# Optimization experiments

Hardware: AMD Instinct MI355X
Metric: run time of the kernel (lower is better)

Reference implementation:

```python
import math
import jax, jax.numpy as jnp
import numpy as np

B = 512
E = 512
C = 70722
M_MARGIN = 0.4
H = 0.333
S = 64.0
T_ALPHA = 1.0
EPS = 1e-3


def setup_inputs() -> dict:
    key = jax.random.key(0)
    k1, k2, k3, k4 = jax.random.split(key, 4)
    embbedings = jax.random.normal(k1, (B, E), dtype=jnp.float32)
    embbedings = embbedings / jnp.linalg.norm(embbedings, axis=1, keepdims=True)
    # feature norms typically ~[10, 30] for face models
    norms = 10.0 + 20.0 * jax.random.uniform(k2, (B, 1), dtype=jnp.float32)
    label = jax.random.randint(k3, (B,), 0, C, dtype=jnp.int64)
    kernel = jax.random.normal(k4, (E, C), dtype=jnp.float32)
    batch_mean = jnp.ones((C,), dtype=jnp.float32) * 20.0
    batch_std = jnp.asarray(10.0, dtype=jnp.float32)
    return {"embbedings": embbedings, "norms": norms, "label": label,
            "kernel": kernel, "batch_mean": batch_mean, "batch_std": batch_std}


def reference(embbedings, norms, label, kernel, batch_mean, batch_std):
    # column-wise l2-normalize the class weight matrix [E, C]
    kernel_norm = kernel / jnp.linalg.norm(kernel, axis=0, keepdims=True)
    cosine = jnp.clip(embbedings @ kernel_norm, -1.0 + EPS, 1.0 - EPS)  # [B, C]
    safe_norms = jnp.clip(norms, 1e-3, 100.0)  # [B, 1]

    # ---- running-stat update (torch.no_grad block) ----
    sn = jax.lax.stop_gradient(safe_norms[:, 0])  # [B]
    sums = jnp.zeros((C,), dtype=sn.dtype).at[label].add(sn)
    counts = jnp.zeros((C,), dtype=sn.dtype).at[label].add(1.0)
    group_mean = sums / jnp.maximum(counts, 1.0)  # per-class batch mean of norms
    new_mean = jnp.where(counts > 0,
                         group_mean * T_ALPHA + (1.0 - T_ALPHA) * batch_mean,
                         batch_mean)
    std = jnp.std(sn, ddof=1)  # torch.std is unbiased
    new_std = std * T_ALPHA + (1.0 - T_ALPHA) * batch_std

    # ---- adaptive margin ----
    margin_scaler = (safe_norms - new_mean[label][:, None]) / (new_std + EPS)
    margin_scaler = jnp.clip(margin_scaler * H, -1.0, 1.0)  # [B, 1]

    oh = jax.nn.one_hot(label, C, dtype=cosine.dtype)  # [B, C]
    g_angular = -M_MARGIN * margin_scaler               # [B, 1]
    theta = jnp.arccos(cosine)
    theta_m = jnp.clip(theta + oh * g_angular, EPS, math.pi - EPS)
    g_add = M_MARGIN + M_MARGIN * margin_scaler         # [B, 1]
    out = (jnp.cos(theta_m) - oh * g_add) * S
    return out
```

## Files before the change

kernel.cpp:

```cpp
#include <hip/hip_runtime.h>
#include <hip/hip_bf16.h>
#include <cstdint>
#include <cstddef>
#include <math.h>

#define B_SZ 512
#define E_SZ 512
#define C_SZ 70722
#define PAD_C 70784
#define M_MARGIN 0.4f
#define H_CONST 0.333f
#define S_CONST 64.0f
#define EPS_F 1e-3f
#define PI_F 3.14159265358979323846f

typedef __attribute__((ext_vector_type(8))) short short8;
typedef __attribute__((ext_vector_type(4))) float f32x4;


__device__ __forceinline__ unsigned short f2bf(float x) {
  __hip_bfloat16 h = __float2bfloat16(x);
  unsigned short u;
  __builtin_memcpy(&u, &h, 2);
  return u;
}

__device__ __forceinline__ void gload_lds16(const void* g, void* l) {
  __builtin_amdgcn_global_load_lds(
      (const __attribute__((address_space(1))) unsigned int*)g,
      (__attribute__((address_space(3))) unsigned int*)l, 16, 0, 0);
}

__device__ __forceinline__ int swzb(int rc) {
  return (((rc & 7) ^ ((rc >> 2) & 7)) << 4);
}

__global__ void k_stats(const float* __restrict__ norms, const int* __restrict__ label,
                        float* __restrict__ ga, float* __restrict__ gadd) {
  __shared__ float sn[B_SZ];
  __shared__ int lab[B_SZ];
  __shared__ float redA[8], redB[8];
  __shared__ float sh_std;

  int t = threadIdx.x;
  float v = norms[t];
  v = fminf(fmaxf(v, 1e-3f), 100.0f);
  sn[t] = v;
  lab[t] = label[t];

  float s1 = v, s2 = v * v;
  #pragma unroll
  for (int o = 32; o > 0; o >>= 1) {
    s1 += __shfl_down(s1, o);
    s2 += __shfl_down(s2, o);
  }
  if ((t & 63) == 0) { redA[t >> 6] = s1; redB[t >> 6] = s2; }
  __syncthreads();
  if (t == 0) {
    float a = 0.f, b = 0.f;
    #pragma unroll
    for (int i = 0; i < 8; ++i) { a += redA[i]; b += redB[i]; }
    float mean = a / (float)B_SZ;
    float var = (b - (float)B_SZ * mean * mean) / (float)(B_SZ - 1);
    sh_std = sqrtf(fmaxf(var, 0.f));
  }
  __syncthreads();
  float stdv = sh_std;

  int myl = lab[t];
  float s = 0.f, cnt = 0.f;
  for (int j = 0; j < B_SZ; ++j) {
    bool m = (lab[j] == myl);
    s += m ? sn[j] : 0.f;
    cnt += m ? 1.f : 0.f;
  }
  float gm = s / fmaxf(cnt, 1.f);
  float ms = (v - gm) / (stdv + EPS_F) * H_CONST;
  ms = fminf(fmaxf(ms, -1.f), 1.f);
  ga[t] = -M_MARGIN * ms;
  gadd[t] = M_MARGIN + M_MARGIN * ms;
}

__global__ void k_cvtA(const float* __restrict__ emb, unsigned short* __restrict__ abf) {
  int i = (blockIdx.x * 256 + threadIdx.x) * 4;
  float4 f = *(const float4*)(emb + i);
  unsigned short u0 = f2bf(f.x), u1 = f2bf(f.y), u2 = f2bf(f.z), u3 = f2bf(f.w);
  unsigned long long pk = (unsigned long long)u0 | ((unsigned long long)u1 << 16) |
                          ((unsigned long long)u2 << 32) | ((unsigned long long)u3 << 48);
  *(unsigned long long*)(abf + i) = pk;
}

__global__ void k_prep(const float* __restrict__ K, float* __restrict__ invn,
                       unsigned short* __restrict__ BT) {
  __shared__ float T[64 * 64];
  __shared__ float part[16][64];

  const int t = threadIdx.x;
  const int c0 = blockIdx.x * 64;
  const int cl = t & 15;
  const int kr = t >> 4;
  const int cq = t >> 2;
  const int kq = t & 3;
  const bool full = (c0 + 64 <= C_SZ);

  float ss0 = 0.f, ss1 = 0.f, ss2 = 0.f, ss3 = 0.f;

  for (int ch = 0; ch < 8; ++ch) {
    if (ch) __syncthreads();
    #pragma unroll
    for (int i = 0; i < 4; ++i) {
      int klo = kr + i * 16;
      int kg = ch * 64 + klo;
      float4 f;
      if (full) {
        f = *(const float4*)(K + (size_t)kg * C_SZ + c0 + cl * 4);
      } else {
        float* fp = (float*)&f;
        #pragma unroll
        for (int j = 0; j < 4; ++j) {
          int c = c0 + cl * 4 + j;
          fp[j] = (c < C_SZ) ? K[(size_t)kg * C_SZ + c] : 0.f;
        }
      }
      ss0 += f.x * f.x; ss1 += f.y * f.y; ss2 += f.z * f.z; ss3 += f.w * f.w;
      int swz = (klo & 7) << 2;
      *(float4*)&T[klo * 64 + ((cl * 4) ^ swz)] = f;
    }
    __syncthreads();
    #pragma unroll
    for (int sub = 0; sub < 2; ++sub) {
      int k8 = sub * 32 + kq * 8;
      short8 v;
      #pragma unroll
      for (int i = 0; i < 8; ++i) {
        v[i] = (short)f2bf(T[(k8 + i) * 64 + (cq ^ (i << 2))]);
      }
      *(short8*)(BT + ((size_t)(c0 + cq) << 9) + ch * 64 + k8) = v;
    }
  }

  __syncthreads();
  part[kr][cl * 4 + 0] = ss0;
  part[kr][cl * 4 + 1] = ss1;
  part[kr][cl * 4 + 2] = ss2;
  part[kr][cl * 4 + 3] = ss3;
  __syncthreads();
  if (t < 64) {
    int c = c0 + t;
    float s = 0.f;
    #pragma unroll
    for (int r = 0; r < 16; ++r) s += part[r][t];
    invn[c] = (c < C_SZ) ? rsqrtf(s) : 0.f;
  }
}

__launch_bounds__(256)
__global__ void k_gemm_fast(const unsigned short* __restrict__ Abf,
                            const unsigned short* __restrict__ BT,
                            const float* __restrict__ invn,
                            const int* __restrict__ label,
                            const float* __restrict__ ga,
                            const float* __restrict__ gadd,
                            float* __restrict__ out) {
  __shared__ __align__(16) unsigned short As[128 * 64];
  __shared__ __align__(16) unsigned short Bs[128 * 64];
  __shared__ int lab_s[128];
  __shared__ float ga_s[128], gadd_s[128];

  const int tid = threadIdx.x;
  const int nwg = gridDim.x;
  int bid = blockIdx.x;

  int q = nwg >> 3, r8 = nwg & 7;
  int xcd = bid & 7, lb = bid >> 3;
  int wg = (xcd < r8 ? xcd * (q + 1) : r8 * (q + 1) + (xcd - r8) * q) + lb;

  const int mt = wg & 3;
  const int nt = wg >> 2;
  const int row0 = mt << 7;
  const int col0 = nt << 7;

  if (tid < 128) {
    int gr = row0 + tid;
    lab_s[tid] = label[gr];
    ga_s[tid] = ga[gr];
    gadd_s[tid] = gadd[gr];
  }

  const int wid = tid >> 6, lane = tid & 63;
  const int wr = wid >> 1, wc = wid & 1;

  f32x4 acc[4][4];
  #pragma unroll
  for (int m = 0; m < 4; ++m)
    #pragma unroll
    for (int n = 0; n < 4; ++n)
      acc[m][n] = f32x4{0.f, 0.f, 0.f, 0.f};

  const int rsub = lane >> 3;
  const int lchunk = lane & 7;

  for (int kt = 0; kt < 8; ++kt) {
    const int kb = kt * 64;
    if (kt) __syncthreads();

    #pragma unroll
    for (int rr = 0; rr < 4; ++rr) {
      int rowblk = wid * 32 + rr * 8;
      int r = rowblk + rsub;
      int s = lchunk ^ ((r & 7) ^ ((r >> 2) & 7));
      gload_lds16(Abf + (size_t)(row0 + r) * 512 + kb + s * 8,
                  (char*)As + rowblk * 128);
      gload_lds16(BT + (size_t)(col0 + r) * 512 + kb + s * 8,
                  (char*)Bs + rowblk * 128);
    }

    __syncthreads();

    #pragma unroll
    for (int ks = 0; ks < 2; ++ks) {
      short8 a[4], b[4];
      #pragma unroll
      for (int m = 0; m < 4; ++m) {
        int row = wr * 64 + m * 16 + (lane & 15);
        int off = (row * 128 + ks * 64 + (lane >> 4) * 16) ^ swzb(row);
        a[m] = *(const short8*)((const char*)As + off);
      }
      #pragma unroll
      for (int n = 0; n < 4; ++n) {
        int c = wc * 64 + n * 16 + (lane & 15);
        int off = (c * 128 + ks * 64 + (lane >> 4) * 16) ^ swzb(c);
        b[n] = *(const short8*)((const char*)Bs + off);
      }
      #pragma unroll
      for (int m = 0; m < 4; ++m)
        #pragma unroll
        for (int n = 0; n < 4; ++n)
          acc[m][n] = __builtin_amdgcn_mfma_f32_16x16x32_bf16(a[m], b[n], acc[m][n], 0, 0, 0);
    }
  }

  float invc[4];
  #pragma unroll
  for (int n = 0; n < 4; ++n)
    invc[n] = invn[col0 + wc * 64 + n * 16 + (lane & 15)];

  #pragma unroll
  for (int m = 0; m < 4; ++m) {
    int rl0 = wr * 64 + m * 16 + ((lane >> 4) << 2);
    #pragma unroll
    for (int n = 0; n < 4; ++n) {
      int cl = wc * 64 + n * 16 + (lane & 15);
      int gc = col0 + cl;
      if (gc >= C_SZ) continue;
      #pragma unroll
      for (int r = 0; r < 4; ++r) {
        int rl = rl0 + r;
        float v = acc[m][n][r] * invc[n];
        v = fminf(fmaxf(v, -1.f + EPS_F), 1.f - EPS_F);
        float res = v * S_CONST;
        if (gc == lab_s[rl]) {
          float th = acosf(v) + ga_s[rl];
          th = fminf(fmaxf(th, EPS_F), PI_F - EPS_F);
          res = (cosf(th) - gadd_s[rl]) * S_CONST;
        }
        out[(size_t)(row0 + rl) * C_SZ + gc] = res;
      }
    }
  }
}


__global__ void k_colnorm(const float* __restrict__ K, float* __restrict__ inv) {
  __shared__ float part[4][64];
  int cl = threadIdx.x & 63;
  int rq = threadIdx.x >> 6;
  int c = blockIdx.x * 64 + cl;
  float s = 0.f;
  if (c < C_SZ) {
    const float* p = K + (size_t)rq * 128 * C_SZ + c;
    #pragma unroll 8
    for (int r = 0; r < 128; ++r) {
      float x = p[(size_t)r * C_SZ];
      s += x * x;
    }
  }
  part[rq][cl] = s;
  __syncthreads();
  if (threadIdx.x < 64) {
    int c2 = blockIdx.x * 64 + threadIdx.x;
    if (c2 < C_SZ) {
      float tt = part[0][threadIdx.x] + part[1][threadIdx.x] +
                 part[2][threadIdx.x] + part[3][threadIdx.x];
      inv[c2] = rsqrtf(tt);
    } else if (c2 < PAD_C) {
      inv[c2] = 0.f;
    }
  }
}

__launch_bounds__(256)
__global__ void k_gemm_fb(const unsigned short* __restrict__ Abf,
                          const float* __restrict__ Kmat,
                          const float* __restrict__ invn,
                          const int* __restrict__ label,
                          const float* __restrict__ ga,
                          const float* __restrict__ gadd,
                          float* __restrict__ out) {
  __shared__ __align__(16) unsigned short As[128 * 64];
  __shared__ __align__(16) unsigned short Bs[128 * 64];
  __shared__ int lab_s[128];
  __shared__ float ga_s[128], gadd_s[128];

  const int tid = threadIdx.x;
  const int nwg = gridDim.x;
  int bid = blockIdx.x;
  int q = nwg >> 3, r8 = nwg & 7;
  int xcd = bid & 7, lb = bid >> 3;
  int wg = (xcd < r8 ? xcd * (q + 1) : r8 * (q + 1) + (xcd - r8) * q) + lb;
  const int mt = wg & 3;
  const int nt = wg >> 2;
  const int row0 = mt << 7;
  const int col0 = nt << 7;

  if (tid < 128) {
    int gr = row0 + tid;
    lab_s[tid] = label[gr];
    ga_s[tid] = ga[gr];
    gadd_s[tid] = gadd[gr];
  }

  const int wid = tid >> 6, lane = tid & 63;
  const int wr = wid >> 1, wc = wid & 1;
  const int cc = tid & 31;
  const int kq = tid >> 5;
  const bool edge = (col0 + 128 > C_SZ);
  float4 inv4 = *(const float4*)(invn + col0 + cc * 4);

  f32x4 acc[4][4];
  #pragma unroll
  for (int m = 0; m < 4; ++m)
    #pragma unroll
    for (int n = 0; n < 4; ++n)
      acc[m][n] = f32x4{0.f, 0.f, 0.f, 0.f};

  const float* Bg = Kmat + col0;

  for (int kt = 0; kt < 8; ++kt) {
    const int kb = kt * 64;
    if (kt) __syncthreads();

    #pragma unroll
    for (int rr = 0; rr < 4; ++rr) {
      int rowblk = wid * 32 + rr * 8;
      int r = rowblk + (lane >> 3);
      int s = (lane & 7) ^ ((r & 7) ^ ((r >> 2) & 7));
      gload_lds16(Abf + (size_t)(row0 + r) * 512 + kb + s * 8, (char*)As + rowblk * 128);
    }

    #pragma unroll
    for (int i = 0; i < 4; ++i) {
      int k = (kq + i * 8) * 2;
      const float* g0 = Bg + (size_t)(kb + k) * C_SZ + cc * 4;
      const float* g1 = g0 + C_SZ;
      float x0[4], x1[4];
      if (!edge) {
        float4 f0 = *(const float4*)g0;
        float4 f1 = *(const float4*)g1;
        x0[0]=f0.x; x0[1]=f0.y; x0[2]=f0.z; x0[3]=f0.w;
        x1[0]=f1.x; x1[1]=f1.y; x1[2]=f1.z; x1[3]=f1.w;
      } else {
        #pragma unroll
        for (int j = 0; j < 4; ++j) {
          int gc = col0 + cc * 4 + j;
          x0[j] = (gc < C_SZ) ? g0[j] : 0.f;
          x1[j] = (gc < C_SZ) ? g1[j] : 0.f;
        }
      }
      #pragma unroll
      for (int j = 0; j < 4; ++j) {
        int c = cc * 4 + j;
        float iv = ((const float*)&inv4)[j];
        unsigned int pk = ((unsigned int)f2bf(x1[j] * iv) << 16) | (unsigned int)f2bf(x0[j] * iv);
        int byte = (c * 128 + k * 2) ^ swzb(c);
        *(unsigned int*)((char*)Bs + byte) = pk;
      }
    }

    __syncthreads();

    #pragma unroll
    for (int ks = 0; ks < 2; ++ks) {
      short8 a[4], b[4];
      #pragma unroll
      for (int m = 0; m < 4; ++m) {
        int row = wr * 64 + m * 16 + (lane & 15);
        int off = (row * 128 + ks * 64 + (lane >> 4) * 16) ^ swzb(row);
        a[m] = *(const short8*)((const char*)As + off);
      }
      #pragma unroll
      for (int n = 0; n < 4; ++n) {
        int c = wc * 64 + n * 16 + (lane & 15);
        int off = (c * 128 + ks * 64 + (lane >> 4) * 16) ^ swzb(c);
        b[n] = *(const short8*)((const char*)Bs + off);
      }
      #pragma unroll
      for (int m = 0; m < 4; ++m)
        #pragma unroll
        for (int n = 0; n < 4; ++n)
          acc[m][n] = __builtin_amdgcn_mfma_f32_16x16x32_bf16(a[m], b[n], acc[m][n], 0, 0, 0);
    }
  }

  #pragma unroll
  for (int m = 0; m < 4; ++m) {
    int rl0 = wr * 64 + m * 16 + ((lane >> 4) << 2);
    #pragma unroll
    for (int n = 0; n < 4; ++n) {
      int cl = wc * 64 + n * 16 + (lane & 15);
      int gc = col0 + cl;
      if (gc >= C_SZ) continue;
      #pragma unroll
      for (int r = 0; r < 4; ++r) {
        int rl = rl0 + r;
        float v = acc[m][n][r];
        v = fminf(fmaxf(v, -1.f + EPS_F), 1.f - EPS_F);
        float res = v * S_CONST;
        if (gc == lab_s[rl]) {
          float th = acosf(v) + ga_s[rl];
          th = fminf(fmaxf(th, EPS_F), PI_F - EPS_F);
          res = (cosf(th) - gadd_s[rl]) * S_CONST;
        }
        out[(size_t)(row0 + rl) * C_SZ + gc] = res;
      }
    }
  }
}

extern "C" void kernel_launch(void* const* d_in, const int* in_sizes, int n_in,
                              void* d_out, int out_size, void* d_ws, size_t ws_size,
                              hipStream_t stream) {
  const float* emb   = (const float*)d_in[0];
  const float* norms = (const float*)d_in[1];
  const int*   label = (const int*)d_in[2];
  const float* kmat  = (const float*)d_in[3];
  float* out = (float*)d_out;

  const size_t NEED_FAST = 73294336;
  char* ws = (char*)d_ws;
  float* invn = (float*)ws;
  float* ga   = (float*)(ws + 283136);
  float* gadd = (float*)(ws + 285184);
  unsigned short* abf = (unsigned short*)(ws + 287232);
  unsigned short* bt  = (unsigned short*)(ws + 811520);

  k_stats<<<1, 512, 0, stream>>>(norms, label, ga, gadd);
  k_cvtA<<<256, 256, 0, stream>>>(emb, abf);

  if (ws_size >= NEED_FAST) {
    k_prep<<<1106, 256, 0, stream>>>(kmat, invn, bt);
    k_gemm_fast<<<2212, 256, 0, stream>>>(abf, bt, invn, label, ga, gadd, out);
  } else {
    k_colnorm<<<1106, 256, 0, stream>>>(kmat, invn);
    k_gemm_fb<<<2212, 256, 0, stream>>>(abf, kmat, invn, label, ga, gadd, out);
  }
}
```

Measured before the change: 150.1 us.

## Triple-buffer LDS with BK=32 prefetch pipeline in fused GEMM kernel

```diff
diff --git a/kernel.cpp b/kernel.cpp
--- a/kernel.cpp
+++ b/kernel.cpp
@@ -162,8 +162,8 @@
                             const float* __restrict__ ga,
                             const float* __restrict__ gadd,
                             float* __restrict__ out) {
-  __shared__ __align__(16) unsigned short As[128 * 64];
-  __shared__ __align__(16) unsigned short Bs[128 * 64];
+  __shared__ __align__(16) unsigned short As[3][128 * 32];
+  __shared__ __align__(16) unsigned short Bs[3][128 * 32];
   __shared__ int lab_s[128];
   __shared__ float ga_s[128], gadd_s[128];
 
@@ -190,6 +190,31 @@
   const int wid = tid >> 6, lane = tid & 63;
   const int wr = wid >> 1, wc = wid & 1;
 
+  const int lr = lane >> 2;
+  const int lc = lane & 3;
+  const int rA0 = wid * 32 + lr;
+  const int rA1 = wid * 32 + 16 + lr;
+  const int sA0 = lc ^ ((rA0 >> 1) & 3);
+  const int sA1 = lc ^ ((rA1 >> 1) & 3);
+  const unsigned short* srcA0 = Abf + (size_t)(row0 + rA0) * 512 + sA0 * 8;
+  const unsigned short* srcA1 = Abf + (size_t)(row0 + rA1) * 512 + sA1 * 8;
+  const unsigned short* srcB0 = BT + (size_t)(col0 + rA0) * 512 + sA0 * 8;
+  const unsigned short* srcB1 = BT + (size_t)(col0 + rA1) * 512 + sA1 * 8;
+  char* const dA0 = (char*)&As[0][0] + (wid * 32) * 64;
+  char* const dB0 = (char*)&Bs[0][0] + (wid * 32) * 64;
+
+  int offA[4], offB[4];
+  #pragma unroll
+  for (int m = 0; m < 4; ++m) {
+    int row = wr * 64 + m * 16 + (lane & 15);
+    offA[m] = row * 64 + (((lane >> 4) ^ ((row >> 1) & 3)) << 4);
+  }
+  #pragma unroll
+  for (int n = 0; n < 4; ++n) {
+    int cr = wc * 64 + n * 16 + (lane & 15);
+    offB[n] = cr * 64 + (((lane >> 4) ^ ((cr >> 1) & 3)) << 4);
+  }
+
   f32x4 acc[4][4];
   #pragma unroll
   for (int m = 0; m < 4; ++m)
@@ -197,48 +222,54 @@
     for (int n = 0; n < 4; ++n)
       acc[m][n] = f32x4{0.f, 0.f, 0.f, 0.f};
 
-  const int rsub = lane >> 3;
-  const int lchunk = lane & 7;
-
-  for (int kt = 0; kt < 8; ++kt) {
-    const int kb = kt * 64;
-    if (kt) __syncthreads();
-
-    #pragma unroll
-    for (int rr = 0; rr < 4; ++rr) {
-      int rowblk = wid * 32 + rr * 8;
-      int r = rowblk + rsub;
-      int s = lchunk ^ ((r & 7) ^ ((r >> 2) & 7));
-      gload_lds16(Abf + (size_t)(row0 + r) * 512 + kb + s * 8,
-                  (char*)As + rowblk * 128);
-      gload_lds16(BT + (size_t)(col0 + r) * 512 + kb + s * 8,
-                  (char*)Bs + rowblk * 128);
-    }
-
-    __syncthreads();
-
-    #pragma unroll
-    for (int ks = 0; ks < 2; ++ks) {
-      short8 a[4], b[4];
-      #pragma unroll
-      for (int m = 0; m < 4; ++m) {
-        int row = wr * 64 + m * 16 + (lane & 15);
-        int off = (row * 128 + ks * 64 + (lane >> 4) * 16) ^ swzb(row);
-        a[m] = *(const short8*)((const char*)As + off);
-      }
-      #pragma unroll
-      for (int n = 0; n < 4; ++n) {
-        int c = wc * 64 + n * 16 + (lane & 15);
-        int off = (c * 128 + ks * 64 + (lane >> 4) * 16) ^ swzb(c);
-        b[n] = *(const short8*)((const char*)Bs + off);
-      }
-      #pragma unroll
-      for (int m = 0; m < 4; ++m)
-        #pragma unroll
-        for (int n = 0; n < 4; ++n)
-          acc[m][n] = __builtin_amdgcn_mfma_f32_16x16x32_bf16(a[m], b[n], acc[m][n], 0, 0, 0);
-    }
-  }
+#define STAGE(nb)                                                        \
+  {                                                                      \
+    char* dA = dA0 + (nb) * 8192;                                        \
+    char* dB = dB0 + (nb) * 8192;                                        \
+    gload_lds16(srcA0, dA);                                              \
+    gload_lds16(srcA1, dA + 1024);                                       \
+    gload_lds16(srcB0, dB);                                              \
+    gload_lds16(srcB1, dB + 1024);                                       \
+    srcA0 += 32; srcA1 += 32; srcB0 += 32; srcB1 += 32;                  \
+  }
+
+  STAGE(0)
+  STAGE(1)
+
+  int bs = 0;
+  for (int kt = 0; kt < 16; ++kt) {
+    if (kt < 15) asm volatile("s_waitcnt vmcnt(4)" ::: "memory");
+    else         asm volatile("s_waitcnt vmcnt(0)" ::: "memory");
+    __builtin_amdgcn_s_barrier();
+    __builtin_amdgcn_sched_barrier(0);
+
+    if (kt < 14) {
+      int nb = bs + 2; if (nb >= 3) nb -= 3;
+      STAGE(nb)
+    }
+
+    const char* pA = (const char*)&As[0][0] + bs * 8192;
+    const char* pB = (const char*)&Bs[0][0] + bs * 8192;
+    short8 a[4], b[4];
+    #pragma unroll
+    for (int m = 0; m < 4; ++m) a[m] = *(const short8*)(pA + offA[m]);
+    #pragma unroll
+    for (int n = 0; n < 4; ++n) b[n] = *(const short8*)(pB + offB[n]);
+
+    asm volatile("s_waitcnt lgkmcnt(0)" ::: "memory");
+    __builtin_amdgcn_sched_barrier(0);
+
+    __builtin_amdgcn_s_setprio(1);
+    #pragma unroll
+    for (int m = 0; m < 4; ++m)
+      #pragma unroll
+      for (int n = 0; n < 4; ++n)
+        acc[m][n] = __builtin_amdgcn_mfma_f32_16x16x32_bf16(a[m], b[n], acc[m][n], 0, 0, 0);
+    __builtin_amdgcn_s_setprio(0);
+
+    bs = (bs == 2) ? 0 : bs + 1;
+  }
+#undef STAGE
 
   float invc[4];
   #pragma unroll
```

Result: slower. 154.7 us (+3.0%).

## Stage GEMM epilogue through LDS for coalesced vectorized nontemporal output stores

Applied to the files above, without the earlier changes.

```diff
diff --git a/kernel.cpp b/kernel.cpp
--- a/kernel.cpp
+++ b/kernel.cpp
@@ -162,8 +162,10 @@
                             const float* __restrict__ ga,
                             const float* __restrict__ gadd,
                             float* __restrict__ out) {
-  __shared__ __align__(16) unsigned short As[128 * 64];
-  __shared__ __align__(16) unsigned short Bs[128 * 64];
+  __shared__ __align__(16) unsigned char smem[64 * 132 * 4];
+  unsigned short* As = (unsigned short*)smem;
+  unsigned short* Bs = (unsigned short*)(smem + 16384);
+  float* cep = (float*)smem;
   __shared__ int lab_s[128];
   __shared__ float ga_s[128], gadd_s[128];
 
@@ -171,9 +173,9 @@
   const int nwg = gridDim.x;
   int bid = blockIdx.x;
 
-  int q = nwg >> 3, r8 = nwg & 7;
+  int q8 = nwg >> 3, r8 = nwg & 7;
   int xcd = bid & 7, lb = bid >> 3;
-  int wg = (xcd < r8 ? xcd * (q + 1) : r8 * (q + 1) + (xcd - r8) * q) + lb;
+  int wg = (xcd < r8 ? xcd * (q8 + 1) : r8 * (q8 + 1) + (xcd - r8) * q8) + lb;
 
   const int mt = wg & 3;
   const int nt = wg >> 2;
@@ -189,6 +191,8 @@
 
   const int wid = tid >> 6, lane = tid & 63;
   const int wr = wid >> 1, wc = wid & 1;
+  const int q = lane >> 4;
+  const int l15 = lane & 15;
 
   f32x4 acc[4][4];
   #pragma unroll
@@ -222,14 +226,14 @@
       short8 a[4], b[4];
       #pragma unroll
       for (int m = 0; m < 4; ++m) {
-        int row = wr * 64 + m * 16 + (lane & 15);
-        int off = (row * 128 + ks * 64 + (lane >> 4) * 16) ^ swzb(row);
+        int row = wr * 64 + m * 16 + l15;
+        int off = (row * 128 + ks * 64 + q * 16) ^ swzb(row);
         a[m] = *(const short8*)((const char*)As + off);
       }
       #pragma unroll
       for (int n = 0; n < 4; ++n) {
-        int c = wc * 64 + n * 16 + (lane & 15);
-        int off = (c * 128 + ks * 64 + (lane >> 4) * 16) ^ swzb(c);
+        int c = wc * 64 + n * 16 + l15;
+        int off = (c * 128 + ks * 64 + q * 16) ^ swzb(c);
         b[n] = *(const short8*)((const char*)Bs + off);
       }
       #pragma unroll
@@ -243,28 +247,52 @@
   float invc[4];
   #pragma unroll
   for (int n = 0; n < 4; ++n)
-    invc[n] = invn[col0 + wc * 64 + n * 16 + (lane & 15)];
-
-  #pragma unroll
-  for (int m = 0; m < 4; ++m) {
-    int rl0 = wr * 64 + m * 16 + ((lane >> 4) << 2);
-    #pragma unroll
-    for (int n = 0; n < 4; ++n) {
-      int cl = wc * 64 + n * 16 + (lane & 15);
-      int gc = col0 + cl;
-      if (gc >= C_SZ) continue;
-      #pragma unroll
-      for (int r = 0; r < 4; ++r) {
-        int rl = rl0 + r;
-        float v = acc[m][n][r] * invc[n];
-        v = fminf(fmaxf(v, -1.f + EPS_F), 1.f - EPS_F);
-        float res = v * S_CONST;
-        if (gc == lab_s[rl]) {
-          float th = acosf(v) + ga_s[rl];
-          th = fminf(fmaxf(th, EPS_F), PI_F - EPS_F);
-          res = (cosf(th) - gadd_s[rl]) * S_CONST;
+    invc[n] = invn[col0 + wc * 64 + n * 16 + l15];
+
+  const int rloc = tid >> 5;
+  const int qd = tid & 31;
+
+  #pragma unroll
+  for (int p = 0; p < 2; ++p) {
+    __syncthreads();
+    if (wr == p) {
+      #pragma unroll
+      for (int m = 0; m < 4; ++m) {
+        #pragma unroll
+        for (int n = 0; n < 4; ++n) {
+          int cl = wc * 64 + n * 16 + l15;
+          int gc = col0 + cl;
+          float iv = invc[n];
+          #pragma unroll
+          for (int r = 0; r < 4; ++r) {
+            int rl = m * 16 + q * 4 + r;
+            float v = acc[m][n][r] * iv;
+            v = fminf(fmaxf(v, -1.f + EPS_F), 1.f - EPS_F);
+            float res = v * S_CONST;
+            if (gc == lab_s[p * 64 + rl]) {
+              float th = acosf(v) + ga_s[p * 64 + rl];
+              th = fminf(fmaxf(th, EPS_F), PI_F - EPS_F);
+              res = (cosf(th) - gadd_s[p * 64 + rl]) * S_CONST;
+            }
+            cep[rl * 132 + cl] = res;
+          }
         }
-        out[(size_t)(row0 + rl) * C_SZ + gc] = res;
+      }
+    }
+    __syncthreads();
+    #pragma unroll
+    for (int it = 0; it < 8; ++it) {
+      int row = rloc + it * 8;
+      f32x4 v = *(const f32x4*)(cep + row * 132 + qd * 4);
+      int grow = row0 + p * 64 + row;
+      int gc0 = col0 + qd * 4;
+      float* dst = out + (size_t)grow * C_SZ + gc0;
+      if (gc0 + 4 <= C_SZ) {
+        __builtin_nontemporal_store(v, (f32x4*)dst);
+      } else {
+        #pragma unroll
+        for (int j = 0; j < 4; ++j)
+          if (gc0 + j < C_SZ) __builtin_nontemporal_store(v[j], dst + j);
       }
     }
   }
```

New measurement: 157.9 us. 1.05x slower.

## Replace 128x128 block GEMM with single-wave 64x64 tiles and pipelined B staging

Applied to the files above, without the earlier changes.

```diff
diff --git a/kernel.cpp b/kernel.cpp
--- a/kernel.cpp
+++ b/kernel.cpp
@@ -8,6 +8,8 @@
 #define E_SZ 512
 #define C_SZ 70722
 #define PAD_C 70784
+#define NTILE 1106
+#define GRID_W (8 * NTILE)
 #define M_MARGIN 0.4f
 #define H_CONST 0.333f
 #define S_CONST 64.0f
@@ -154,41 +156,37 @@
   }
 }
 
-__launch_bounds__(256)
-__global__ void k_gemm_fast(const unsigned short* __restrict__ Abf,
+__launch_bounds__(64, 4)
+__global__ void k_gemm_wave(const unsigned short* __restrict__ Abf,
                             const unsigned short* __restrict__ BT,
                             const float* __restrict__ invn,
                             const int* __restrict__ label,
                             const float* __restrict__ ga,
                             const float* __restrict__ gadd,
                             float* __restrict__ out) {
-  __shared__ __align__(16) unsigned short As[128 * 64];
-  __shared__ __align__(16) unsigned short Bs[128 * 64];
-  __shared__ int lab_s[128];
-  __shared__ float ga_s[128], gadd_s[128];
-
-  const int tid = threadIdx.x;
-  const int nwg = gridDim.x;
+  __shared__ __align__(16) unsigned short Bs[64 * 64];
+
+  const int lane = threadIdx.x;
+  const int q = lane >> 4;
+  const int l15 = lane & 15;
+
   int bid = blockIdx.x;
-
-  int q = nwg >> 3, r8 = nwg & 7;
-  int xcd = bid & 7, lb = bid >> 3;
-  int wg = (xcd < r8 ? xcd * (q + 1) : r8 * (q + 1) + (xcd - r8) * q) + lb;
-
-  const int mt = wg & 3;
-  const int nt = wg >> 2;
-  const int row0 = mt << 7;
-  const int col0 = nt << 7;
-
-  if (tid < 128) {
-    int gr = row0 + tid;
-    lab_s[tid] = label[gr];
-    ga_s[tid] = ga[gr];
-    gadd_s[tid] = gadd[gr];
-  }
-
-  const int wid = tid >> 6, lane = tid & 63;
-  const int wr = wid >> 1, wc = wid & 1;
+  int wg = (bid & 7) * NTILE + (bid >> 3);
+  const int mt = wg & 7;
+  const int nt = wg >> 3;
+  const int row0 = mt << 6;
+  const int col0 = nt << 6;
+
+  const char* aP[4];
+  #pragma unroll
+  for (int m = 0; m < 4; ++m)
+    aP[m] = (const char*)(Abf + (size_t)(row0 + m * 16 + l15) * 512 + q * 8);
+
+  const int br = lane >> 3, bch = lane & 7;
+  const char* const bsrc0 =
+      (const char*)(BT + (size_t)(col0 + br) * 512 + ((bch ^ (br & 3)) * 8));
+
+  const char* const bfb = (const char*)Bs + l15 * 128 + ((q ^ (l15 & 3)) << 4);
 
   f32x4 acc[4][4];
   #pragma unroll
@@ -197,74 +195,100 @@
     for (int n = 0; n < 4; ++n)
       acc[m][n] = f32x4{0.f, 0.f, 0.f, 0.f};
 
-  const int rsub = lane >> 3;
-  const int lchunk = lane & 7;
-
-  for (int kt = 0; kt < 8; ++kt) {
-    const int kb = kt * 64;
-    if (kt) __syncthreads();
-
-    #pragma unroll
-    for (int rr = 0; rr < 4; ++rr) {
-      int rowblk = wid * 32 + rr * 8;
-      int r = rowblk + rsub;
-      int s = lchunk ^ ((r & 7) ^ ((r >> 2) & 7));
-      gload_lds16(Abf + (size_t)(row0 + r) * 512 + kb + s * 8,
-                  (char*)As + rowblk * 128);
-      gload_lds16(BT + (size_t)(col0 + r) * 512 + kb + s * 8,
-                  (char*)Bs + rowblk * 128);
-    }
-
-    __syncthreads();
-
-    #pragma unroll
-    for (int ks = 0; ks < 2; ++ks) {
-      short8 a[4], b[4];
-      #pragma unroll
-      for (int m = 0; m < 4; ++m) {
-        int row = wr * 64 + m * 16 + (lane & 15);
-        int off = (row * 128 + ks * 64 + (lane >> 4) * 16) ^ swzb(row);
-        a[m] = *(const short8*)((const char*)As + off);
-      }
+  short8 a0[4], a1[4], b[4];
+
+#define BSTAGE(KT)                                                           \
+  { const char* bs_ = bsrc0 + (KT) * 128; char* d_ = (char*)Bs;              \
+    _Pragma("unroll")                                                        \
+    for (int i_ = 0; i_ < 8; ++i_) {                                         \
+      gload_lds16(bs_, d_); bs_ += 8192; d_ += 1024; } }
+
+#define ALOAD(AR, KT, KS)                                                    \
+  { _Pragma("unroll")                                                        \
+    for (int m_ = 0; m_ < 4; ++m_)                                           \
+      AR[m_] = *(const short8*)(aP[m_] + (KT) * 128 + (KS) * 64); }
+
+  BSTAGE(0)
+  ALOAD(a0, 0, 0)
+  ALOAD(a1, 0, 1)
+  asm volatile("s_waitcnt vmcnt(8)" ::: "memory");
+  __builtin_amdgcn_sched_barrier(0);
+
+#define GSTEP(KT, ISLAST)                                                    \
+  {                                                                          \
+    _Pragma("unroll")                                                        \
+    for (int n_ = 0; n_ < 4; ++n_)                                           \
+      b[n_] = *(const short8*)(bfb + n_ * 2048);                   \
+    asm volatile("s_waitcnt lgkmcnt(0) vmcnt(4)" ::: "memory");              \
+    __builtin_amdgcn_sched_barrier(0);                                       \
+    __builtin_amdgcn_s_setprio(1);                                           \
+    _Pragma("unroll")                                                        \
+    for (int m_ = 0; m_ < 4; ++m_)                                           \
+      _Pragma("unroll")                                                      \
+      for (int n_ = 0; n_ < 4; ++n_)                                         \
+        acc[m_][n_] = __builtin_amdgcn_mfma_f32_16x16x32_bf16(               \
+            a0[m_], b[n_], acc[m_][n_], 0, 0, 0);                            \
+    __builtin_amdgcn_s_setprio(0);                                           \
+    __builtin_amdgcn_sched_barrier(0);                                       \
+    _Pragma("unroll")                                                        \
+    for (int n_ = 0; n_ < 4; ++n_)                                           \
+      b[n_] = *(const short8*)(bfb + n_ * 2048 + 64);              \
+    asm volatile("s_waitcnt lgkmcnt(0)" ::: "memory");                       \
+    __builtin_amdgcn_sched_barrier(0);                                       \
+    if (!(ISLAST)) { BSTAGE((KT) + 1) }                                      \
+    __builtin_amdgcn_sched_barrier(0);                                       \
+    if (!(ISLAST)) { asm volatile("s_waitcnt vmcnt(8)" ::: "memory"); }      \
+    else           { asm volatile("s_waitcnt vmcnt(0)" ::: "memory"); }      \
+    __builtin_amdgcn_sched_barrier(0);                                       \
+    __builtin_amdgcn_s_setprio(1);                                           \
+    _Pragma("unroll")                                                        \
+    for (int m_ = 0; m_ < 4; ++m_)                                           \
+      _Pragma("unroll")                                                      \
+      for (int n_ = 0; n_ < 4; ++n_)                                         \
+        acc[m_][n_] = __builtin_amdgcn_mfma_f32_16x16x32_bf16(               \
+            a1[m_], b[n_], acc[m_][n_], 0, 0, 0);                            \
+    __builtin_amdgcn_s_setprio(0);                                           \
+    __builtin_amdgcn_sched_barrier(0);                                       \
+    if (!(ISLAST)) {                                                         \
+      ALOAD(a0, (KT) + 1, 0)                                                 \
+      ALOAD(a1, (KT) + 1, 1)                                                 \
+      __builtin_amdgcn_sched_barrier(0);                                     \
+      asm volatile("s_waitcnt vmcnt(8)" ::: "memory");     \
+      __builtin_amdgcn_sched_barrier(0);                                     \
+    }                                                                        \
+  }
+
+  GSTEP(0, 0) GSTEP(1, 0) GSTEP(2, 0) GSTEP(3, 0)
+  GSTEP(4, 0) GSTEP(5, 0) GSTEP(6, 0) GSTEP(7, 1)
+#undef GSTEP
+#undef ALOAD
+#undef BSTAGE
+
+  float invc[4];
+  #pragma unroll
+  for (int n = 0; n < 4; ++n)
+    invc[n] = invn[col0 + n * 16 + l15];
+
+  #pragma unroll
+  for (int m = 0; m < 4; ++m) {
+    #pragma unroll
+    for (int r = 0; r < 4; ++r) {
+      int grow = row0 + m * 16 + q * 4 + r;
+      int lab = label[grow];
+      float gav = ga[grow], gadv = gadd[grow];
       #pragma unroll
       for (int n = 0; n < 4; ++n) {
-        int c = wc * 64 + n * 16 + (lane & 15);
-        int off = (c * 128 + ks * 64 + (lane >> 4) * 16) ^ swzb(c);
-        b[n] = *(const short8*)((const char*)Bs + off);
-      }
-      #pragma unroll
-      for (int m = 0; m < 4; ++m)
-        #pragma unroll
-        for (int n = 0; n < 4; ++n)
-          acc[m][n] = __builtin_amdgcn_mfma_f32_16x16x32_bf16(a[m], b[n], acc[m][n], 0, 0, 0);
-    }
-  }
-
-  float invc[4];
-  #pragma unroll
-  for (int n = 0; n < 4; ++n)
-    invc[n] = invn[col0 + wc * 64 + n * 16 + (lane & 15)];
-
-  #pragma unroll
-  for (int m = 0; m < 4; ++m) {
-    int rl0 = wr * 64 + m * 16 + ((lane >> 4) << 2);
-    #pragma unroll
-    for (int n = 0; n < 4; ++n) {
-      int cl = wc * 64 + n * 16 + (lane & 15);
-      int gc = col0 + cl;
-      if (gc >= C_SZ) continue;
-      #pragma unroll
-      for (int r = 0; r < 4; ++r) {
-        int rl = rl0 + r;
+        int gc = col0 + n * 16 + l15;
+        if (gc >= C_SZ) continue;
         float v = acc[m][n][r] * invc[n];
         v = fminf(fmaxf(v, -1.f + EPS_F), 1.f - EPS_F);
         float res = v * S_CONST;
-        if (gc == lab_s[rl]) {
-          float th = acosf(v) + ga_s[rl];
+        if (gc == lab) {
+          float th = acosf(v) + gav;
           th = fminf(fmaxf(th, EPS_F), PI_F - EPS_F);
-          res = (cosf(th) - gadd_s[rl]) * S_CONST;
+          res = (cosf(th) - gadv) * S_CONST;
         }
-        out[(size_t)(row0 + rl) * C_SZ + gc] = res;
+        out[(size_t)grow * C_SZ + gc] = res;
       }
     }
   }
@@ -459,7 +483,7 @@
 
   if (ws_size >= NEED_FAST) {
     k_prep<<<1106, 256, 0, stream>>>(kmat, invn, bt);
-    k_gemm_fast<<<2212, 256, 0, stream>>>(abf, bt, invn, label, ga, gadd, out);
+    k_gemm_wave<<<GRID_W, 64, 0, stream>>>(abf, bt, invn, label, ga, gadd, out);
   } else {
     k_colnorm<<<1106, 256, 0, stream>>>(kmat, invn);
     k_gemm_fb<<<2212, 256, 0, stream>>>(abf, kmat, invn, label, ga, gadd, out);
```

Result: slower. 184.2 us (+22.7%).
